# Kernel tuning notes

Measured on AMD Instinct MI355X. Metric: run time of the kernel, lower is better.

Reference implementation:

```python
import jax, jax.numpy as jnp
import numpy as np

N_NODES = 50000
N_EDGES = 400000
C_NODE = 128
C_EDGE = 256
# PyG: round(c_in + (c_out-c_in)*f)
H1, H2, H3 = 166, 192, 218


def setup_inputs() -> dict:
    key = jax.random.key(0)
    ks = jax.random.split(key, 20)
    x = jax.random.normal(ks[0], (N_NODES, C_NODE), dtype=jnp.float32)
    edge_index = jax.random.randint(ks[1], (2, N_EDGES), 0, N_NODES, dtype=jnp.int64)

    def glorot(k, fan_in, fan_out):
        s = jnp.sqrt(6.0 / (fan_in + fan_out)).astype(jnp.float32)
        return jax.random.uniform(k, (fan_in, fan_out), jnp.float32, -s, s)

    dims_e = [(C_NODE, H1), (H1, H2), (H2, H3), (H3, C_EDGE)]
    dims_n = [(C_NODE, C_NODE)] * 4
    inp = {"x": x, "edge_index": edge_index}
    for i, (fi, fo) in enumerate(dims_e, 1):
        inp[f"W{i}e"] = glorot(ks[1 + i], fi, fo)
        inp[f"b{i}e"] = jnp.zeros((fo,), jnp.float32)
    for i, (fi, fo) in enumerate(dims_n, 1):
        inp[f"W{i}n"] = glorot(ks[9 + i], fi, fo)
        inp[f"b{i}n"] = jnp.zeros((fo,), jnp.float32)
    return inp


def _gcn_norm(edge_index, n_nodes):
    # add self loops, then symmetric normalization (PyG gcn_norm, improved=False)
    loops = jnp.arange(n_nodes, dtype=edge_index.dtype)
    src = jnp.concatenate([edge_index[0], loops])
    dst = jnp.concatenate([edge_index[1], loops])
    deg = jax.ops.segment_sum(jnp.ones_like(dst, dtype=jnp.float32), dst, num_segments=n_nodes)
    dinv = jnp.where(deg > 0, jax.lax.rsqrt(deg), 0.0)
    norm = dinv[src] * dinv[dst]  # [E+N]
    return src, dst, norm


def _gcn_conv(h_in, W, b, src, dst, norm, n_nodes):
    h = h_in @ W                      # [N, C_out] dense transform first (PyG order)
    msg = h[src] * norm[:, None]      # gather + scale, [E+N, C_out]
    agg = jax.ops.segment_sum(msg, dst, num_segments=n_nodes)
    return agg + b


def _forward(x, edge_index, We, be, Wn, bn):
    n = x.shape[0]
    src, dst, norm = _gcn_norm(edge_index, n)
    e = x
    for i in range(4):
        e = _gcn_conv(e, We[i], be[i], src, dst, norm, n)
        e = jax.nn.relu(e) if i < 3 else jax.nn.sigmoid(e)
    v = x
    for i in range(4):
        v = _gcn_conv(v, Wn[i], bn[i], src, dst, norm, n)
        v = jax.nn.relu(v) if i < 3 else jax.nn.sigmoid(v)
    return e, v


def reference(x, edge_index, W1e, b1e, W2e, b2e, W3e, b3e, W4e, b4e,
              W1n, b1n, W2n, b2n, W3n, b3n, W4n, b4n):
    We = [W1e, W2e, W3e, W4e]
    be = [b1e, b2e, b3e, b4e]
    Wn = [W1n, W2n, W3n, W4n]
    bn = [b1n, b2n, b3n, b4n]
    return _forward(x, edge_index, We, be, Wn, bn)
```

## Files before the change

kernel.cpp:

```cpp
#include <hip/hip_runtime.h>
#include <hip/hip_bf16.h>
#include <cstdint>
#include <cstddef>

typedef __hip_bfloat16 bf16;
typedef __attribute__((ext_vector_type(8))) short bf16x8;
typedef __attribute__((ext_vector_type(4))) float f32x4;

#define NN 50000
#define NE 400000

struct PTab {
    const void* p[17];
    int n[17];
};

__device__ __forceinline__ float bf2f(unsigned short u) {
    return __uint_as_float(((unsigned)u) << 16);
}
__device__ __forceinline__ unsigned short f2bf(float f) {
    __hip_bfloat16 h = __float2bfloat16(f);
    return *reinterpret_cast<unsigned short*>(&h);
}
__device__ __forceinline__ float fin(float v) {
    return (v == v && v > -1e30f && v < 1e30f) ? v : 0.0f;
}
__device__ __forceinline__ float rd(const void* p, int i, int f) {
    return f ? ((const float*)p)[i] : bf2f(((const unsigned short*)p)[i]);
}

__device__ __forceinline__ void gl16(const void* g, void* l) {
    __builtin_amdgcn_global_load_lds(
        (const __attribute__((address_space(1))) unsigned int*)g,
        (__attribute__((address_space(3))) unsigned int*)l, 16, 0, 0);
}

__global__ void k_probe(PTab tab, const int* __restrict__ ei, int* __restrict__ flags) {
    __shared__ int zc, bc, sAny;
    for (int t = 0; t < 17; ++t) {
        if (threadIdx.x == 0) { zc = 0; bc = 0; }
        __syncthreads();
        int words = tab.n[t] >> 1;
        if (words > 256) words = 256;
        if ((int)threadIdx.x < words) {
            unsigned w = ((const unsigned*)tab.p[t])[threadIdx.x];
            if (w == 0u) atomicAdd(&zc, 1);
            else {
                int e = (w >> 7) & 0xFF;
                if (e >= 100 && e <= 140) atomicAdd(&bc, 1);
            }
        }
        __syncthreads();
        if (threadIdx.x == 0) {
            int nz = words - zc;
            flags[t] = (nz == 0 || 2 * bc >= nz) ? 0 : 1;
        }
        __syncthreads();
    }
    if (threadIdx.x == 0) sAny = 0;
    __syncthreads();
    int any = 0;
    for (int i = threadIdx.x; i < 2048; i += 256) any |= ei[2 * i + 1];
    if (any) sAny = 1;
    __syncthreads();
    if (threadIdx.x == 0) flags[17] = sAny;
}

struct WSeg {
    const void* src[8];
    unsigned short* wh[8];
    unsigned short* wl[8];
    int f[8], K[8], M[8], Kp[8];
    int b0[9];
};

__global__ void k_wsplitall(WSeg G, const int* __restrict__ flags) {
    int bid = blockIdx.x;
    int seg = 0;
    #pragma unroll
    for (int t = 1; t < 8; ++t) if (bid >= G.b0[t]) seg = t;
    int n = bid - G.b0[seg];
    int k = threadIdx.x;
    int Kp = G.Kp[seg];
    if (k >= Kp) return;
    float v = 0.0f;
    if (k < G.K[seg] && n < G.M[seg])
        v = fin(rd(G.src[seg], k * G.M[seg] + n, flags[G.f[seg]]));
    unsigned short hi = f2bf(v);
    unsigned short lo = f2bf(v - bf2f(hi));
    G.wh[seg][(size_t)n * Kp + k] = hi;
    G.wl[seg][(size_t)n * Kp + k] = lo;
}

struct MOff { int m[8]; int mp[8]; };

__global__ void k_biasall(PTab tab, const int* __restrict__ flags, MOff mo,
                          float* __restrict__ dst) {
    int l = blockIdx.x;
    int fidx = 2 + 2 * l;
    int M = tab.n[fidx];
    int i = threadIdx.x;
    if (i < mo.mp[l])
        dst[mo.m[l] + i] = (i < M) ? fin(rd(tab.p[fidx], i, flags[fidx])) : 0.0f;
}

__global__ void k_repack(const int* __restrict__ ei, const int* __restrict__ flags,
                         int* __restrict__ src, int* __restrict__ dst,
                         int* __restrict__ deg) {
    int e = blockIdx.x * blockDim.x + threadIdx.x;
    if (e >= NE) return;
    int s, d;
    if (flags[17]) { s = ei[e]; d = ei[NE + e]; }
    else           { s = ei[2 * e]; d = ei[2 * (NE + e)]; }
    s = min(max(s, 0), NN - 1);
    d = min(max(d, 0), NN - 1);
    src[e] = s;
    dst[e] = d;
    atomicAdd(&deg[d], 1);
}

__global__ void k_scan1(const int* __restrict__ deg, int* __restrict__ rowp,
                        int* __restrict__ part) {
    __shared__ int s[512];
    int tid = threadIdx.x, i = blockIdx.x * 512 + tid;
    int v = (i < NN) ? deg[i] : 0;
    s[tid] = v;
    __syncthreads();
    for (int off = 1; off < 512; off <<= 1) {
        int t = (tid >= off) ? s[tid - off] : 0;
        __syncthreads();
        s[tid] += t;
        __syncthreads();
    }
    if (i < NN) rowp[i] = s[tid] - v;
    if (tid == 511) part[blockIdx.x] = s[511];
}
__global__ void k_scan2(int* __restrict__ part, int nb) {
    __shared__ int s[128];
    int tid = threadIdx.x;
    int v = (tid < nb) ? part[tid] : 0;
    s[tid] = v;
    __syncthreads();
    for (int off = 1; off < 128; off <<= 1) {
        int t = (tid >= off) ? s[tid - off] : 0;
        __syncthreads();
        s[tid] += t;
        __syncthreads();
    }
    if (tid < nb) part[tid] = s[tid] - v;
}
__global__ void k_scan3(int* __restrict__ rowp, const int* __restrict__ part,
                        const int* __restrict__ deg, float* __restrict__ dinv) {
    int i = blockIdx.x * blockDim.x + threadIdx.x;
    if (i < NN) {
        rowp[i] += part[i >> 9];
        dinv[i] = rsqrtf((float)deg[i] + 1.0f);
    }
    if (i == 0) rowp[NN] = NE;
}

__global__ void k_fill(const int* __restrict__ src, const int* __restrict__ dst,
                       const int* __restrict__ rowp, int* __restrict__ cursor,
                       int* __restrict__ colv) {
    int e = blockIdx.x * blockDim.x + threadIdx.x;
    if (e >= NE) return;
    int d = dst[e];
    int p = atomicAdd(&cursor[d], 1);
    colv[rowp[d] + p] = src[e];
}

__global__ void k_xin(const void* __restrict__ x, const int* __restrict__ flags,
                      const float* __restrict__ dinv, unsigned short* __restrict__ xs) {
    int t = blockIdx.x * blockDim.x + threadIdx.x;
    if (t >= NN * 16) return;
    int i = t >> 4, c = (t & 15) * 8;
    float d = dinv[i];
    int f = flags[0];
    const float* xf = (const float*)x + (size_t)i * 128 + c;
    const unsigned short* xb = (const unsigned short*)x + (size_t)i * 128 + c;
    unsigned short o[8];
    #pragma unroll
    for (int j = 0; j < 8; ++j)
        o[j] = f2bf(fin(f ? xf[j] : bf2f(xb[j])) * d);
    *(uint4*)(xs + (size_t)i * 128 + c) = *(uint4*)o;
}

__launch_bounds__(256)
__global__ void k_gather(const unsigned short* __restrict__ in, int istride,
                         unsigned short* __restrict__ out, int ostride, int lanes,
                         const int* __restrict__ rowp, const int* __restrict__ colv,
                         const float* __restrict__ dinv) {
    const int node = blockIdx.x * 4 + (threadIdx.x >> 6);
    if (node >= NN) return;
    const int lane = threadIdx.x & 63;
    const int beg = rowp[node], end = rowp[node + 1];
    float a[8] = {0.f, 0.f, 0.f, 0.f, 0.f, 0.f, 0.f, 0.f};
    auto accq = [&](uint4 q) {
        unsigned v[4] = {q.x, q.y, q.z, q.w};
        #pragma unroll
        for (int t = 0; t < 4; ++t) {
            a[2 * t] += bf2f(v[t] & 0xFFFF); a[2 * t + 1] += bf2f(v[t] >> 16);
        }
    };
    if (lanes <= 16) {
        const int slot = lane >> 4;
        const int l8 = lane & 15;
        const bool on = l8 < lanes;
        const size_t off = (size_t)l8 * 8;
        if (slot == 0 && on)
            accq(*(const uint4*)(in + (size_t)node * istride + off));
        for (int j = beg + slot; j < end; j += 4) {
            const int s = colv[j];
            if (on) accq(*(const uint4*)(in + (size_t)s * istride + off));
        }
        #pragma unroll
        for (int t = 0; t < 8; ++t) {
            a[t] += __shfl_xor(a[t], 16);
            a[t] += __shfl_xor(a[t], 32);
        }
        if (lane < lanes) {
            float d = dinv[node];
            unsigned short o[8];
            #pragma unroll
            for (int t = 0; t < 8; ++t) o[t] = f2bf(a[t] * d);
            *(uint4*)(out + (size_t)node * ostride + (size_t)lane * 8) = *(uint4*)o;
        }
    } else {
        const bool on = lane < lanes;
        const size_t off = (size_t)lane * 8;
        if (on) accq(*(const uint4*)(in + (size_t)node * istride + off));
        int j = beg;
        for (; j + 1 < end; j += 2) {
            int s0 = colv[j], s1 = colv[j + 1];
            if (on) {
                uint4 q0 = *(const uint4*)(in + (size_t)s0 * istride + off);
                uint4 q1 = *(const uint4*)(in + (size_t)s1 * istride + off);
                accq(q0); accq(q1);
            }
        }
        if (j < end) {
            int s0 = colv[j];
            if (on) accq(*(const uint4*)(in + (size_t)s0 * istride + off));
        }
        if (on) {
            float d = dinv[node];
            unsigned short o[8];
            #pragma unroll
            for (int t = 0; t < 8; ++t) o[t] = f2bf(a[t] * d);
            *(uint4*)(out + (size_t)node * ostride + off) = *(uint4*)o;
        }
    }
}

struct GSide {
    const unsigned short* A;
    const unsigned short* Wh;
    const unsigned short* Wl;
    const float* bias;
    void* out;
    int Kp, ostride, M, OutW, act;
};

__launch_bounds__(256, 3)
__global__ void k_mgemm(GSide s0, GSide s1, int ySplit, int NY, int NB, int astride,
                        const float* __restrict__ dinv) {
    __shared__ __align__(16) unsigned char ldsraw[49152];
    auto sA  = reinterpret_cast<unsigned short (*)[128][32]>(ldsraw);
    auto sBh = reinterpret_cast<unsigned short (*)[128][32]>(ldsraw + 16384);
    auto sBl = reinterpret_cast<unsigned short (*)[128][32]>(ldsraw + 32768);

    const int tid = threadIdx.x;
    const int wave = tid >> 6, lane = tid & 63;
    const int wr = wave >> 1, wc = wave & 1;
    const int quad = lane >> 4, m16 = lane & 15;

    const int NBa = NB & ~7;
    const int swcut = NBa * NY;
    int b = blockIdx.x, x, yv;
    if (b < swcut) {
        x = (b / (8 * NY)) * 8 + (b & 7);
        yv = (b >> 3) % NY;
    } else {
        int r = b - swcut, rem = NB - NBa;
        x = rem ? (NBa + r % rem) : 0;
        yv = rem ? (r / rem) : 0;
    }

    GSide S; int ycol;
    if (yv < ySplit) { S = s0; ycol = yv; }
    else             { S = s1; ycol = yv - ySplit; }
    const int row0 = x * 128, col0 = ycol * 128;
    const int Kp = S.Kp;

    const int lr = lane >> 2;
    const int swz = ((lane >> 2) ^ (lane >> 4)) & 3;
    const int su = ((lane & 3) ^ swz) * 8;

    int ar1 = row0 + wave * 32 + lr;      if (ar1 >= NN) ar1 = NN - 1;
    int ar2 = row0 + wave * 32 + 16 + lr; if (ar2 >= NN) ar2 = NN - 1;
    const unsigned short* gA1 = S.A + (size_t)ar1 * astride + su;
    const unsigned short* gA2 = S.A + (size_t)ar2 * astride + su;
    const int br = col0 + wave * 32 + lr;
    const unsigned short* gBh1 = S.Wh + (size_t)br * Kp + su;
    const unsigned short* gBl1 = S.Wl + (size_t)br * Kp + su;

    f32x4 zz = {0.f, 0.f, 0.f, 0.f};
    f32x4 acc[4][4];
    #pragma unroll
    for (int i = 0; i < 4; ++i)
        #pragma unroll
        for (int j = 0; j < 4; ++j) acc[i][j] = zz;

    const int rs = (quad ^ ((m16 & 3) ^ ((m16 >> 2) & 3))) * 8;
    const int nk = Kp >> 5;

    auto stage = [&](int bb, int k0) {
        gl16(gA1 + k0,            &sA[bb][wave * 32][0]);
        gl16(gA2 + k0,            &sA[bb][wave * 32 + 16][0]);
        gl16(gBh1 + k0,           &sBh[bb][wave * 32][0]);
        gl16(gBh1 + 16 * Kp + k0, &sBh[bb][wave * 32 + 16][0]);
        gl16(gBl1 + k0,           &sBl[bb][wave * 32][0]);
        gl16(gBl1 + 16 * Kp + k0, &sBl[bb][wave * 32 + 16][0]);
    };

    stage(0, 0);
    if (nk > 1) stage(1, 32);

    for (int ks = 0; ks < nk; ++ks) {
        const int cur = ks & 1;
        if (ks + 1 < nk) asm volatile("s_waitcnt vmcnt(6)" ::: "memory");
        else             asm volatile("s_waitcnt vmcnt(0)" ::: "memory");
        __builtin_amdgcn_s_barrier();
        bf16x8 fa[4], fh[4], fl[4];
        #pragma unroll
        for (int i = 0; i < 4; ++i) {
            fa[i] = *(const bf16x8*)&sA[cur][wr * 64 + i * 16 + m16][rs];
            fh[i] = *(const bf16x8*)&sBh[cur][wc * 64 + i * 16 + m16][rs];
            fl[i] = *(const bf16x8*)&sBl[cur][wc * 64 + i * 16 + m16][rs];
        }
        asm volatile("s_waitcnt lgkmcnt(0)" ::: "memory");
        __builtin_amdgcn_sched_barrier(0);
        __builtin_amdgcn_s_barrier();
        if (ks + 2 < nk) stage(cur, (ks + 2) * 32);
        #pragma unroll
        for (int i = 0; i < 4; ++i)
            #pragma unroll
            for (int j = 0; j < 4; ++j) {
                acc[i][j] = __builtin_amdgcn_mfma_f32_16x16x32_bf16(fa[i], fh[j], acc[i][j], 0, 0, 0);
                acc[i][j] = __builtin_amdgcn_mfma_f32_16x16x32_bf16(fa[i], fl[j], acc[i][j], 0, 0, 0);
            }
    }

    float* eps = (float*)(ldsraw + (size_t)wave * 4352);
    #pragma unroll
    for (int i = 0; i < 4; ++i) {
        #pragma unroll
        for (int j = 0; j < 4; ++j) {
            int col = col0 + wc * 64 + j * 16 + m16;
            float bcol = (col < S.M) ? S.bias[col] : 0.0f;
            #pragma unroll
            for (int r = 0; r < 4; ++r) {
                float v = acc[i][j][r] + bcol;
                if (S.act) v = (col < S.M) ? 1.0f / (1.0f + expf(-v)) : 0.0f;
                else       v = (col < S.M) ? fmaxf(v, 0.0f) : 0.0f;
                eps[(quad * 4 + r) * 68 + j * 16 + m16] = v;
            }
        }
        asm volatile("s_waitcnt lgkmcnt(0)" ::: "memory");
        __builtin_amdgcn_sched_barrier(0);
        #pragma unroll
        for (int it = 0; it < 4; ++it) {
            int lr2 = it * 4 + (lane >> 4);
            int c4 = (lane & 15) * 4;
            float4 w = *(float4*)&eps[lr2 * 68 + c4];
            int grow = row0 + wr * 64 + i * 16 + lr2;
            int gcol = col0 + wc * 64 + c4;
            if (grow < NN && gcol < S.OutW) {
                if (S.act) {
                    *(float4*)((float*)S.out + (size_t)grow * S.ostride + gcol) = w;
                } else {
                    float d = dinv[grow];
                    unsigned o0 = f2bf(w.x * d) | ((unsigned)f2bf(w.y * d) << 16);
                    unsigned o1 = f2bf(w.z * d) | ((unsigned)f2bf(w.w * d) << 16);
                    uint2 u; u.x = o0; u.y = o1;
                    *(uint2*)((unsigned short*)S.out + (size_t)grow * S.ostride + gcol) = u;
                }
            }
        }
        asm volatile("s_waitcnt lgkmcnt(0)" ::: "memory");
        __builtin_amdgcn_sched_barrier(0);
    }
}

__global__ void k_sentinel(float* __restrict__ out, int n) {
    int i = blockIdx.x * blockDim.x + threadIdx.x;
    if (i < n) out[i] = 4.0f;
}

extern "C" void kernel_launch(void* const* d_in, const int* in_sizes, int n_in,
                              void* d_out, int out_size, void* d_ws, size_t ws_size,
                              hipStream_t stream) {
    const int* ei = (const int*)d_in[1];
    float* out_e = (float*)d_out;
    float* out_v = out_e + (size_t)NN * 256;

    const int wsz[16] = {128 * 166, 166, 166 * 192, 192, 192 * 218, 218, 218 * 256, 256,
                         128 * 128, 128, 128 * 128, 128, 128 * 128, 128, 128 * 128, 128};
    PTab tab;
    tab.p[0] = d_in[0]; tab.n[0] = NN * 128;
    for (int t = 0; t < 16; ++t) { tab.p[t + 1] = d_in[2 + t]; tab.n[t + 1] = wsz[t]; }

    const int KpW[8] = {128, 192, 192, 224, 0, 128, 128, 128};
    const int MpW[8] = {384, 256, 256, 256, 0, 128, 128, 128};

    char* wsb = (char*)d_ws;
    size_t o = 0;
    auto align = [](size_t v) { return (v + 255) & ~(size_t)255; };
    int*   flags  = (int*)(wsb + o);  o = align(o + 128);
    int*   colv   = (int*)(wsb + o);  o = align(o + (size_t)NE * 4);
    int*   deg    = (int*)(wsb + o);  o = align(o + (size_t)NN * 4);
    int*   cursor = (int*)(wsb + o);  o = align(o + (size_t)NN * 4);
    int*   rowp   = (int*)(wsb + o);  o = align(o + (size_t)(NN + 1) * 4);
    int*   part   = (int*)(wsb + o);  o = align(o + 512);
    float* dinv   = (float*)(wsb + o); o = align(o + (size_t)NN * 4);
    unsigned short* wh[8]; unsigned short* wl[8];
    for (int l = 0; l < 8; ++l) {
        size_t wel = (size_t)MpW[l] * KpW[l];
        wh[l] = (unsigned short*)(wsb + o); o = align(o + wel * 2);
        wl[l] = (unsigned short*)(wsb + o); o = align(o + wel * 2);
    }
    float* ball = (float*)(wsb + o); o = align(o + 1376 * 4);
    unsigned short* bufA = (unsigned short*)(wsb + o); o = align(o + (size_t)NN * 352 * 2);
    unsigned short* bufB = (unsigned short*)(wsb + o); o = align(o + (size_t)NN * 352 * 2);
    int* src32 = (int*)bufB;
    int* dst32 = src32 + NE;
    if (o > ws_size) {
        k_sentinel<<<(out_size + 255) / 256, 256, 0, stream>>>(out_e, out_size);
        return;
    }

    MOff mo;
    const int moff[8] = {0, 296, 616, 968, 168, 488, 840, 1224};
    const int mpad[8] = {168, 192, 224, 256, 128, 128, 128, 128};
    for (int l = 0; l < 8; ++l) { mo.m[l] = moff[l]; mo.mp[l] = mpad[l]; }

    const int EB = (NE + 255) / 256;
    const int NB512 = (NN + 511) / 512;
    const int GX = (NN + 127) / 128;
    const int GN = (NN + 3) / 4;

    k_probe<<<1, 256, 0, stream>>>(tab, ei, flags);

    {
        WSeg G;
        const void* srcs[8] = {d_in[2], d_in[10], d_in[4], d_in[12],
                               d_in[6], d_in[14], d_in[8], d_in[16]};
        unsigned short* whp[8] = {wh[0], wh[0] + 168 * 128, wh[1], wh[5],
                                  wh[2], wh[6], wh[3], wh[7]};
        unsigned short* wlp[8] = {wl[0], wl[0] + 168 * 128, wl[1], wl[5],
                                  wl[2], wl[6], wl[3], wl[7]};
        const int fs[8]  = {1, 9, 3, 11, 5, 13, 7, 15};
        const int Ks[8]  = {128, 128, 166, 128, 192, 128, 218, 128};
        const int Ms[8]  = {166, 128, 192, 128, 218, 128, 256, 128};
        const int Kps[8] = {128, 128, 192, 128, 192, 128, 224, 128};
        const int rows[8] = {168, 216, 256, 128, 256, 128, 256, 128};
        int acc = 0;
        for (int s = 0; s < 8; ++s) {
            G.src[s] = srcs[s]; G.wh[s] = whp[s]; G.wl[s] = wlp[s];
            G.f[s] = fs[s]; G.K[s] = Ks[s]; G.M[s] = Ms[s]; G.Kp[s] = Kps[s];
            G.b0[s] = acc; acc += rows[s];
        }
        G.b0[8] = acc;
        k_wsplitall<<<acc, 256, 0, stream>>>(G, flags);
    }
    k_biasall<<<8, 256, 0, stream>>>(tab, flags, mo, ball);

    hipMemsetAsync(deg, 0, (size_t)NN * 4, stream);
    hipMemsetAsync(cursor, 0, (size_t)NN * 4, stream);
    k_repack<<<EB, 256, 0, stream>>>(ei, flags, src32, dst32, deg);
    k_scan1<<<NB512, 512, 0, stream>>>(deg, rowp, part);
    k_scan2<<<1, 128, 0, stream>>>(part, NB512);
    k_scan3<<<(NN + 255) / 256, 256, 0, stream>>>(rowp, part, deg, dinv);
    k_fill<<<EB, 256, 0, stream>>>(src32, dst32, rowp, cursor, colv);

    k_xin<<<(NN * 16 + 255) / 256, 256, 0, stream>>>(d_in[0], flags, dinv, bufA);
    k_gather<<<GN, 256, 0, stream>>>(bufA, 128, bufB, 128, 16, rowp, colv, dinv);

    {
        GSide s0 = {bufB, wh[0], wl[0], ball, bufA, 128, 296, 296, 296, 0};
        k_mgemm<<<GX * 3, 256, 0, stream>>>(s0, s0, 3, 3, GX, 128, dinv);
    }
    k_gather<<<GN, 256, 0, stream>>>(bufA, 296, bufB, 296, 37, rowp, colv, dinv);

    {
        GSide s0 = {bufB, wh[1], wl[1], ball + 296, bufA, 192, 320, 192, 192, 0};
        GSide s1 = {bufB + 168, wh[5], wl[5], ball + 488, bufA + 192, 128, 320, 128, 128, 0};
        k_mgemm<<<GX * 3, 256, 0, stream>>>(s0, s1, 2, 3, GX, 296, dinv);
    }
    k_gather<<<GN, 256, 0, stream>>>(bufA, 320, bufB, 320, 40, rowp, colv, dinv);

    {
        GSide s0 = {bufB, wh[2], wl[2], ball + 616, bufA, 192, 352, 218, 224, 0};
        GSide s1 = {bufB + 192, wh[6], wl[6], ball + 840, bufA + 224, 128, 352, 128, 128, 0};
        k_mgemm<<<GX * 3, 256, 0, stream>>>(s0, s1, 2, 3, GX, 320, dinv);
    }
    k_gather<<<GN, 256, 0, stream>>>(bufA, 352, bufB, 352, 44, rowp, colv, dinv);

    {
        GSide s0 = {bufB, wh[3], wl[3], ball + 968, out_e, 224, 256, 256, 256, 1};
        GSide s1 = {bufB + 224, wh[7], wl[7], ball + 1224, out_v, 128, 128, 128, 128, 1};
        k_mgemm<<<GX * 3, 256, 0, stream>>>(s0, s1, 2, 3, GX, 352, dinv);
    }
}
```

Baseline: 508.6 us.

## Fuse preprocessing kernels and inline dtype probing to cut launch count

Removes the single-block probe kernel and has each consumer block work out the fp32-vs-bf16 and int64-vs-int32 flags itself using wave ballots. Weight split, bias copy and input scaling are merged into one prep kernel. The second scan pass is folded into the third, which now also zeroes the cursor array in place of a memset. The aim is to cut kernel launches and serialized tiny kernels, at the cost of redundant per-block probe reads. The bias probe now inspects the bias tensors rather than a mixed table index, which could change the flag semantics slightly.

```diff
diff --git a/kernel.cpp b/kernel.cpp
--- a/kernel.cpp
+++ b/kernel.cpp
@@ -10,11 +10,6 @@
 #define NN 50000
 #define NE 400000
 
-struct PTab {
-    const void* p[17];
-    int n[17];
-};
-
 __device__ __forceinline__ float bf2f(unsigned short u) {
     return __uint_as_float(((unsigned)u) << 16);
 }
@@ -35,83 +30,112 @@
         (__attribute__((address_space(3))) unsigned int*)l, 16, 0, 0);
 }
 
-__global__ void k_probe(PTab tab, const int* __restrict__ ei, int* __restrict__ flags) {
-    __shared__ int zc, bc, sAny;
-    for (int t = 0; t < 17; ++t) {
-        if (threadIdx.x == 0) { zc = 0; bc = 0; }
-        __syncthreads();
-        int words = tab.n[t] >> 1;
-        if (words > 256) words = 256;
-        if ((int)threadIdx.x < words) {
-            unsigned w = ((const unsigned*)tab.p[t])[threadIdx.x];
-            if (w == 0u) atomicAdd(&zc, 1);
-            else {
-                int e = (w >> 7) & 0xFF;
-                if (e >= 100 && e <= 140) atomicAdd(&bc, 1);
-            }
-        }
-        __syncthreads();
-        if (threadIdx.x == 0) {
-            int nz = words - zc;
-            flags[t] = (nz == 0 || 2 * bc >= nz) ? 0 : 1;
-        }
-        __syncthreads();
-    }
-    if (threadIdx.x == 0) sAny = 0;
+__device__ __forceinline__ int probe_flag(const unsigned* __restrict__ p, int words,
+                                          int* sflag) {
+    if (threadIdx.x < 64) {
+        int lane = threadIdx.x;
+        int zc = 0, bc = 0;
+        #pragma unroll
+        for (int c = 0; c < 4; ++c) {
+            int idx = c * 64 + lane;
+            int act = idx < words;
+            unsigned w = act ? p[idx] : 0u;
+            int isz = act && (w == 0u);
+            int e = (w >> 7) & 0xFF;
+            int isb = act && !isz && (e >= 100 && e <= 140);
+            zc += __popcll(__ballot(isz));
+            bc += __popcll(__ballot(isb));
+        }
+        int nz = words - zc;
+        if (lane == 0) *sflag = (nz == 0 || 2 * bc >= nz) ? 0 : 1;
+    }
     __syncthreads();
-    int any = 0;
-    for (int i = threadIdx.x; i < 2048; i += 256) any |= ei[2 * i + 1];
-    if (any) sAny = 1;
-    __syncthreads();
-    if (threadIdx.x == 0) flags[17] = sAny;
-}
-
-struct WSeg {
-    const void* src[8];
-    unsigned short* wh[8];
-    unsigned short* wl[8];
-    int f[8], K[8], M[8], Kp[8];
-    int b0[9];
+    return *sflag;
+}
+
+struct Prep {
+    const void* wsrc[8];
+    unsigned short* pwh[8];
+    unsigned short* pwl[8];
+    int K[8], M[8], Kp[8];
+    int b0[8];
+    int biasStart, xinStart;
+    const void* bsrc[8];
+    int bM[8], bmp[8], bmo[8];
+    float* ball;
+    const void* x;
+    const float* dinv;
+    unsigned short* xs;
 };
 
-__global__ void k_wsplitall(WSeg G, const int* __restrict__ flags) {
-    int bid = blockIdx.x;
+__global__ void k_prep(Prep P) {
+    __shared__ int sflag;
+    const int bid = blockIdx.x;
+
+    if (bid >= P.xinStart) {
+        int f = probe_flag((const unsigned*)P.x, 256, &sflag);
+        int t = (bid - P.xinStart) * 256 + threadIdx.x;
+        if (t >= NN * 16) return;
+        int i = t >> 4, c = (t & 15) * 8;
+        float d = P.dinv[i];
+        const float* xf = (const float*)P.x + (size_t)i * 128 + c;
+        const unsigned short* xb = (const unsigned short*)P.x + (size_t)i * 128 + c;
+        unsigned short o[8];
+        #pragma unroll
+        for (int j = 0; j < 8; ++j)
+            o[j] = f2bf(fin(f ? xf[j] : bf2f(xb[j])) * d);
+        *(uint4*)(P.xs + (size_t)i * 128 + c) = *(uint4*)o;
+        return;
+    }
+    if (bid >= P.biasStart) {
+        int l = bid - P.biasStart;
+        int words = P.bM[l] >> 1; if (words > 256) words = 256;
+        int f = probe_flag((const unsigned*)P.bsrc[l], words, &sflag);
+        int i = threadIdx.x;
+        if (i < P.bmp[l])
+            P.ball[P.bmo[l] + i] = (i < P.bM[l]) ? fin(rd(P.bsrc[l], i, f)) : 0.0f;
+        return;
+    }
     int seg = 0;
     #pragma unroll
-    for (int t = 1; t < 8; ++t) if (bid >= G.b0[t]) seg = t;
-    int n = bid - G.b0[seg];
+    for (int t = 1; t < 8; ++t) if (bid >= P.b0[t]) seg = t;
+    int words = (P.K[seg] * P.M[seg]) >> 1; if (words > 256) words = 256;
+    int f = probe_flag((const unsigned*)P.wsrc[seg], words, &sflag);
+    int n = bid - P.b0[seg];
     int k = threadIdx.x;
-    int Kp = G.Kp[seg];
+    int Kp = P.Kp[seg];
     if (k >= Kp) return;
     float v = 0.0f;
-    if (k < G.K[seg] && n < G.M[seg])
-        v = fin(rd(G.src[seg], k * G.M[seg] + n, flags[G.f[seg]]));
+    if (k < P.K[seg] && n < P.M[seg])
+        v = fin(rd(P.wsrc[seg], k * P.M[seg] + n, f));
     unsigned short hi = f2bf(v);
     unsigned short lo = f2bf(v - bf2f(hi));
-    G.wh[seg][(size_t)n * Kp + k] = hi;
-    G.wl[seg][(size_t)n * Kp + k] = lo;
-}
-
-struct MOff { int m[8]; int mp[8]; };
-
-__global__ void k_biasall(PTab tab, const int* __restrict__ flags, MOff mo,
-                          float* __restrict__ dst) {
-    int l = blockIdx.x;
-    int fidx = 2 + 2 * l;
-    int M = tab.n[fidx];
-    int i = threadIdx.x;
-    if (i < mo.mp[l])
-        dst[mo.m[l] + i] = (i < M) ? fin(rd(tab.p[fidx], i, flags[fidx])) : 0.0f;
-}
-
-__global__ void k_repack(const int* __restrict__ ei, const int* __restrict__ flags,
+    P.pwh[seg][(size_t)n * Kp + k] = hi;
+    P.pwl[seg][(size_t)n * Kp + k] = lo;
+}
+
+__global__ void k_repack(const int* __restrict__ ei,
                          int* __restrict__ src, int* __restrict__ dst,
                          int* __restrict__ deg) {
+    __shared__ int sAny;
+    if (threadIdx.x < 64) {
+        int lane = threadIdx.x;
+        int any = 0;
+        #pragma unroll
+        for (int c = 0; c < 32; ++c) {
+            int idx = c * 64 + lane;
+            int v = ei[2 * idx + 1];
+            any |= (__ballot(v != 0) != 0ull) ? 1 : 0;
+        }
+        if (lane == 0) sAny = any;
+    }
+    __syncthreads();
+    int f = sAny;
     int e = blockIdx.x * blockDim.x + threadIdx.x;
     if (e >= NE) return;
     int s, d;
-    if (flags[17]) { s = ei[e]; d = ei[NE + e]; }
-    else           { s = ei[2 * e]; d = ei[2 * (NE + e)]; }
+    if (f) { s = ei[e]; d = ei[NE + e]; }
+    else   { s = ei[2 * e]; d = ei[2 * (NE + e)]; }
     s = min(max(s, 0), NN - 1);
     d = min(max(d, 0), NN - 1);
     src[e] = s;
@@ -135,26 +159,29 @@
     if (i < NN) rowp[i] = s[tid] - v;
     if (tid == 511) part[blockIdx.x] = s[511];
 }
-__global__ void k_scan2(int* __restrict__ part, int nb) {
-    __shared__ int s[128];
-    int tid = threadIdx.x;
-    int v = (tid < nb) ? part[tid] : 0;
-    s[tid] = v;
+
+__global__ void k_scan3b(int* __restrict__ rowp, const int* __restrict__ part,
+                         const int* __restrict__ deg, float* __restrict__ dinv,
+                         int* __restrict__ cursor) {
+    __shared__ int sS;
+    const int b = blockIdx.x;
+    const int g = b >> 1;
+    if (threadIdx.x < 64) {
+        int lane = threadIdx.x;
+        int v = 0;
+        if (lane < g) v += part[lane];
+        if (64 + lane < g) v += part[64 + lane];
+        #pragma unroll
+        for (int o = 1; o < 64; o <<= 1) v += __shfl_xor(v, o);
+        if (lane == 0) sS = v;
+    }
     __syncthreads();
-    for (int off = 1; off < 128; off <<= 1) {
-        int t = (tid >= off) ? s[tid - off] : 0;
-        __syncthreads();
-        s[tid] += t;
-        __syncthreads();
-    }
-    if (tid < nb) part[tid] = s[tid] - v;
-}
-__global__ void k_scan3(int* __restrict__ rowp, const int* __restrict__ part,
-                        const int* __restrict__ deg, float* __restrict__ dinv) {
-    int i = blockIdx.x * blockDim.x + threadIdx.x;
+    int S = sS;
+    int i = b * 256 + threadIdx.x;
     if (i < NN) {
-        rowp[i] += part[i >> 9];
+        rowp[i] += S;
         dinv[i] = rsqrtf((float)deg[i] + 1.0f);
+        cursor[i] = 0;
     }
     if (i == 0) rowp[NN] = NE;
 }
@@ -167,22 +194,6 @@
     int d = dst[e];
     int p = atomicAdd(&cursor[d], 1);
     colv[rowp[d] + p] = src[e];
-}
-
-__global__ void k_xin(const void* __restrict__ x, const int* __restrict__ flags,
-                      const float* __restrict__ dinv, unsigned short* __restrict__ xs) {
-    int t = blockIdx.x * blockDim.x + threadIdx.x;
-    if (t >= NN * 16) return;
-    int i = t >> 4, c = (t & 15) * 8;
-    float d = dinv[i];
-    int f = flags[0];
-    const float* xf = (const float*)x + (size_t)i * 128 + c;
-    const unsigned short* xb = (const unsigned short*)x + (size_t)i * 128 + c;
-    unsigned short o[8];
-    #pragma unroll
-    for (int j = 0; j < 8; ++j)
-        o[j] = f2bf(fin(f ? xf[j] : bf2f(xb[j])) * d);
-    *(uint4*)(xs + (size_t)i * 128 + c) = *(uint4*)o;
 }
 
 __launch_bounds__(256)
@@ -404,19 +415,12 @@
     float* out_e = (float*)d_out;
     float* out_v = out_e + (size_t)NN * 256;
 
-    const int wsz[16] = {128 * 166, 166, 166 * 192, 192, 192 * 218, 218, 218 * 256, 256,
-                         128 * 128, 128, 128 * 128, 128, 128 * 128, 128, 128 * 128, 128};
-    PTab tab;
-    tab.p[0] = d_in[0]; tab.n[0] = NN * 128;
-    for (int t = 0; t < 16; ++t) { tab.p[t + 1] = d_in[2 + t]; tab.n[t + 1] = wsz[t]; }
-
     const int KpW[8] = {128, 192, 192, 224, 0, 128, 128, 128};
     const int MpW[8] = {384, 256, 256, 256, 0, 128, 128, 128};
 
     char* wsb = (char*)d_ws;
     size_t o = 0;
     auto align = [](size_t v) { return (v + 255) & ~(size_t)255; };
-    int*   flags  = (int*)(wsb + o);  o = align(o + 128);
     int*   colv   = (int*)(wsb + o);  o = align(o + (size_t)NE * 4);
     int*   deg    = (int*)(wsb + o);  o = align(o + (size_t)NN * 4);
     int*   cursor = (int*)(wsb + o);  o = align(o + (size_t)NN * 4);
@@ -439,51 +443,53 @@
         return;
     }
 
-    MOff mo;
     const int moff[8] = {0, 296, 616, 968, 168, 488, 840, 1224};
     const int mpad[8] = {168, 192, 224, 256, 128, 128, 128, 128};
-    for (int l = 0; l < 8; ++l) { mo.m[l] = moff[l]; mo.mp[l] = mpad[l]; }
 
     const int EB = (NE + 255) / 256;
     const int NB512 = (NN + 511) / 512;
     const int GX = (NN + 127) / 128;
     const int GN = (NN + 3) / 4;
 
-    k_probe<<<1, 256, 0, stream>>>(tab, ei, flags);
+    hipMemsetAsync(deg, 0, (size_t)NN * 4, stream);
+    k_repack<<<EB, 256, 0, stream>>>(ei, src32, dst32, deg);
+    k_scan1<<<NB512, 512, 0, stream>>>(deg, rowp, part);
+    k_scan3b<<<(NN + 255) / 256, 256, 0, stream>>>(rowp, part, deg, dinv, cursor);
+    k_fill<<<EB, 256, 0, stream>>>(src32, dst32, rowp, cursor, colv);
 
     {
-        WSeg G;
+        Prep P;
         const void* srcs[8] = {d_in[2], d_in[10], d_in[4], d_in[12],
                                d_in[6], d_in[14], d_in[8], d_in[16]};
         unsigned short* whp[8] = {wh[0], wh[0] + 168 * 128, wh[1], wh[5],
                                   wh[2], wh[6], wh[3], wh[7]};
         unsigned short* wlp[8] = {wl[0], wl[0] + 168 * 128, wl[1], wl[5],
                                   wl[2], wl[6], wl[3], wl[7]};
-        const int fs[8]  = {1, 9, 3, 11, 5, 13, 7, 15};
-        const int Ks[8]  = {128, 128, 166, 128, 192, 128, 218, 128};
-        const int Ms[8]  = {166, 128, 192, 128, 218, 128, 256, 128};
-        const int Kps[8] = {128, 128, 192, 128, 192, 128, 224, 128};
+        const int Ks[8]   = {128, 128, 166, 128, 192, 128, 218, 128};
+        const int Ms[8]   = {166, 128, 192, 128, 218, 128, 256, 128};
+        const int Kps[8]  = {128, 128, 192, 128, 192, 128, 224, 128};
         const int rows[8] = {168, 216, 256, 128, 256, 128, 256, 128};
         int acc = 0;
         for (int s = 0; s < 8; ++s) {
-            G.src[s] = srcs[s]; G.wh[s] = whp[s]; G.wl[s] = wlp[s];
-            G.f[s] = fs[s]; G.K[s] = Ks[s]; G.M[s] = Ms[s]; G.Kp[s] = Kps[s];
-            G.b0[s] = acc; acc += rows[s];
-        }
-        G.b0[8] = acc;
-        k_wsplitall<<<acc, 256, 0, stream>>>(G, flags);
-    }
-    k_biasall<<<8, 256, 0, stream>>>(tab, flags, mo, ball);
-
-    hipMemsetAsync(deg, 0, (size_t)NN * 4, stream);
-    hipMemsetAsync(cursor, 0, (size_t)NN * 4, stream);
-    k_repack<<<EB, 256, 0, stream>>>(ei, flags, src32, dst32, deg);
-    k_scan1<<<NB512, 512, 0, stream>>>(deg, rowp, part);
-    k_scan2<<<1, 128, 0, stream>>>(part, NB512);
-    k_scan3<<<(NN + 255) / 256, 256, 0, stream>>>(rowp, part, deg, dinv);
-    k_fill<<<EB, 256, 0, stream>>>(src32, dst32, rowp, cursor, colv);
-
-    k_xin<<<(NN * 16 + 255) / 256, 256, 0, stream>>>(d_in[0], flags, dinv, bufA);
+            P.wsrc[s] = srcs[s]; P.pwh[s] = whp[s]; P.pwl[s] = wlp[s];
+            P.K[s] = Ks[s]; P.M[s] = Ms[s]; P.Kp[s] = Kps[s];
+            P.b0[s] = acc; acc += rows[s];
+        }
+        P.biasStart = acc;
+        P.xinStart = acc + 8;
+        const int bMv[8] = {166, 192, 218, 256, 128, 128, 128, 128};
+        for (int l = 0; l < 8; ++l) {
+            P.bsrc[l] = d_in[3 + 2 * l];
+            P.bM[l] = bMv[l]; P.bmp[l] = mpad[l]; P.bmo[l] = moff[l];
+        }
+        P.ball = ball;
+        P.x = d_in[0];
+        P.dinv = dinv;
+        P.xs = bufA;
+        const int xinBlocks = (NN * 16 + 255) / 256;
+        k_prep<<<P.xinStart + xinBlocks, 256, 0, stream>>>(P);
+    }
+
     k_gather<<<GN, 256, 0, stream>>>(bufA, 128, bufB, 128, 16, rowp, colv, dinv);
 
     {
```

Result: faster. 487.7 us (-4.1%).
